# Kernel tuning notes

Measured on AMD Instinct MI355X. Metric: run time of the kernel, lower is better.

Reference implementation:

```python
import jax, jax.numpy as jnp
import numpy as np


def setup_inputs() -> dict:
    key = jax.random.key(0)
    k1, k2, k3, k4, k5 = jax.random.split(key, 5)
    B, ENS, XDIM, YDIM = 8, 256, 8192, 256
    return {
        "Ens_ten": jax.random.normal(k1, (B, ENS, XDIM), dtype=jnp.float32),
        "H": jax.random.normal(k2, (XDIM, YDIM), dtype=jnp.float32),
        "y_true_mean": jax.random.normal(k3, (1, YDIM), dtype=jnp.float32),
        "y_true_std": jax.random.normal(k4, (1, YDIM), dtype=jnp.float32),
        "noise": jax.random.normal(k5, (B, YDIM, ENS), dtype=jnp.float32),
    }


def reference(Ens_ten, H, y_true_mean, y_true_std, noise):
    # Ens_ten: [b, ens, xdim]; H: [xdim, ydim]
    b, ens, xdim = Ens_ten.shape
    Y = jnp.einsum('bex,xy->bey', Ens_ten, H)          # observation_func (linear)
    x_m = jnp.mean(Ens_ten, axis=1, keepdims=True)     # [b,1,xdim]
    y_m = jnp.mean(Y, axis=1, keepdims=True)           # [b,1,ydim]
    Xc = jnp.swapaxes(Ens_ten - x_m, 1, 2)             # [b,xdim,ens]
    Yc = jnp.swapaxes(Y - y_m, 1, 2)                   # [b,ydim,ens]
    C_xy = jnp.einsum('bxe,bye->bxy', Xc, Yc) / ens    # [b,xdim,ydim]
    C_yy = jnp.einsum('bue,bve->buv', Yc, Yc) / ens    # [b,ydim,ydim]
    R = jnp.diag(jnp.square(y_true_std)[0])            # [ydim,ydim], broadcasts over batch
    A = R + C_yy                                       # [b,ydim,ydim]
    # torch.linalg.solve(A, C_xy, left=False): K = C_xy @ inv(A)
    K = jnp.swapaxes(
        jnp.linalg.solve(jnp.swapaxes(A, 1, 2), jnp.swapaxes(C_xy, 1, 2)), 1, 2
    )                                                  # [b,xdim,ydim]
    R_2 = noise * jnp.square(y_true_std)[:, :, None]   # [b,ydim,ens]
    innov = y_true_mean[:, :, None] - Yc + R_2         # [b,ydim,ens]
    update = jnp.einsum('bxy,bye->bxe', K, innov)      # [b,xdim,ens]
    return Ens_ten + jnp.swapaxes(update, 1, 2)
```

## Files before the change

### kernel.cpp

```cpp
#include <hip/hip_runtime.h>

#define ENSN 256
#define XDIM 8192
#define YD 256
#define BATCH 8

#define OFF_Y   0
#define OFF_YC  524288
#define OFF_AUG 1048576
#define OFF_W   2097152
#define OFF_XM  2621440

typedef __attribute__((ext_vector_type(4))) short short4v;
typedef __attribute__((ext_vector_type(8))) short short8v;
typedef __attribute__((ext_vector_type(4))) float float4v;

__device__ __forceinline__ unsigned short f2bf_rne(float x) {
    unsigned u = __float_as_uint(x);
    u += 0x7FFFu + ((u >> 16) & 1u);
    return (unsigned short)(u >> 16);
}

__global__ __launch_bounds__(256) void k1_colmean(const float* __restrict__ E,
                                                  float* __restrict__ xm) {
    int x = blockIdx.x * 256 + threadIdx.x;
    int b = blockIdx.y;
    const float* p = E + (size_t)b * ENSN * XDIM + x;
    float s = 0.f;
    #pragma unroll 8
    for (int e = 0; e < ENSN; e++) s += p[(size_t)e * XDIM];
    xm[b * XDIM + x] = s * (1.0f / ENSN);
}

__global__ __launch_bounds__(256) void kc_h(const float* __restrict__ H,
                                            short* __restrict__ Hthi,
                                            short* __restrict__ Htlo) {
    __shared__ float T[64][65];
    int k0 = blockIdx.x * 64, n0 = blockIdx.y * 64;
    int tid = threadIdx.x;
    int c = tid & 63, g = tid >> 6;
    #pragma unroll
    for (int p = 0; p < 16; p++)
        T[g + p * 4][c] = H[(size_t)(k0 + g + p * 4) * YD + n0 + c];
    __syncthreads();
    #pragma unroll
    for (int p = 0; p < 16; p++) {
        int nn = g + p * 4;
        float v = T[c][nn];
        unsigned short h = f2bf_rne(v);
        float hf = __uint_as_float(((unsigned)h) << 16);
        unsigned short l2 = f2bf_rne(v - hf);
        Hthi[(size_t)(n0 + nn) * XDIM + k0 + c] = (short)h;
        Htlo[(size_t)(n0 + nn) * XDIM + k0 + c] = (short)l2;
    }
}

#define EST 40
#define BST 40

__global__ __launch_bounds__(512, 2) void k2m_ygemm(const float* __restrict__ E,
                                                    const short* __restrict__ Hthi,
                                                    const short* __restrict__ Htlo,
                                                    float* __restrict__ Y) {
    __shared__ __align__(16) short Ehi[64 * EST];
    __shared__ __align__(16) short Elo[64 * EST];
    __shared__ __align__(16) short Bhi[256 * BST];
    __shared__ __align__(16) short Blo[256 * BST];
    int tid = threadIdx.x;
    int lane = tid & 63;
    int w = tid >> 6;
    int m0 = blockIdx.x * 64;
    int kb0 = blockIdx.y * 512;
    int wr = (w & 1) * 32;
    int wc = (w >> 1) * 64;
    float4v acc[8];
    #pragma unroll
    for (int i = 0; i < 8; i++) acc[i] = (float4v){0.f, 0.f, 0.f, 0.f};

    int erow = tid >> 3, ecol = (tid & 7) * 4;
    int brow4 = tid >> 2, bch = (tid & 3) * 8;
    int fr = lane & 15, fg = lane >> 4;

    for (int s = 0; s < 16; s++) {
        int kb = kb0 + s * 32;
        float4 ev = *(const float4*)&E[(size_t)(m0 + erow) * XDIM + kb + ecol];
        float vv[4] = {ev.x, ev.y, ev.z, ev.w};
        short4v hi4, lo4;
        #pragma unroll
        for (int j = 0; j < 4; j++) {
            unsigned short h = f2bf_rne(vv[j]);
            float hf = __uint_as_float(((unsigned)h) << 16);
            unsigned short l2 = f2bf_rne(vv[j] - hf);
            hi4[j] = (short)h; lo4[j] = (short)l2;
        }
        *(short4v*)&Ehi[erow * EST + ecol] = hi4;
        *(short4v*)&Elo[erow * EST + ecol] = lo4;
        #pragma unroll
        for (int pass = 0; pass < 2; pass++) {
            int rowb = brow4 + pass * 128;
            *(short8v*)&Bhi[rowb * BST + bch] =
                *(const short8v*)&Hthi[(size_t)rowb * XDIM + kb + bch];
            *(short8v*)&Blo[rowb * BST + bch] =
                *(const short8v*)&Htlo[(size_t)rowb * XDIM + kb + bch];
        }
        __syncthreads();
        short8v ah[2], al[2], bhf[4], blf[4];
        #pragma unroll
        for (int ti = 0; ti < 2; ti++) {
            ah[ti] = *(const short8v*)&Ehi[(wr + ti * 16 + fr) * EST + fg * 8];
            al[ti] = *(const short8v*)&Elo[(wr + ti * 16 + fr) * EST + fg * 8];
        }
        #pragma unroll
        for (int tj = 0; tj < 4; tj++) {
            bhf[tj] = *(const short8v*)&Bhi[(wc + tj * 16 + fr) * BST + fg * 8];
            blf[tj] = *(const short8v*)&Blo[(wc + tj * 16 + fr) * BST + fg * 8];
        }
        #pragma unroll
        for (int ti = 0; ti < 2; ti++)
            #pragma unroll
            for (int tj = 0; tj < 4; tj++) {
                int a = ti * 4 + tj;
                acc[a] = __builtin_amdgcn_mfma_f32_16x16x32_bf16(ah[ti], bhf[tj], acc[a], 0, 0, 0);
                acc[a] = __builtin_amdgcn_mfma_f32_16x16x32_bf16(ah[ti], blf[tj], acc[a], 0, 0, 0);
                acc[a] = __builtin_amdgcn_mfma_f32_16x16x32_bf16(al[ti], bhf[tj], acc[a], 0, 0, 0);
            }
        __syncthreads();
    }
    #pragma unroll
    for (int ti = 0; ti < 2; ti++)
        #pragma unroll
        for (int tj = 0; tj < 4; tj++)
            #pragma unroll
            for (int q = 0; q < 4; q++) {
                int row = m0 + wr + ti * 16 + fg * 4 + q;
                int col = wc + tj * 16 + fr;
                atomicAdd(&Y[row * YD + col], acc[ti * 4 + tj][q]);
            }
}

__global__ __launch_bounds__(256) void k3_center(const float* __restrict__ Y,
                                                 const float* __restrict__ ytm,
                                                 const float* __restrict__ ystd,
                                                 const float* __restrict__ noise,
                                                 float* __restrict__ Yc,
                                                 float* __restrict__ aug) {
    int b = blockIdx.y, tid = threadIdx.x;
    int y0 = blockIdx.x * 64;
    __shared__ float red[4][64];
    __shared__ float ym[64], tms[64], s2[64];
    __shared__ float T[64][65];
    int yl = tid & 63, q = tid >> 6;
    float s = 0.f;
    for (int e = q * 64; e < q * 64 + 64; e++)
        s += Y[(size_t)(b * ENSN + e) * YD + y0 + yl];
    red[q][yl] = s;
    __syncthreads();
    if (tid < 64) {
        ym[tid] = (red[0][tid] + red[1][tid] + red[2][tid] + red[3][tid]) * (1.0f / ENSN);
        float sd = ystd[y0 + tid];
        s2[tid] = sd * sd;
        tms[tid] = ytm[y0 + tid];
    }
    __syncthreads();
    for (int e0 = 0; e0 < ENSN; e0 += 64) {
        #pragma unroll
        for (int p = 0; p < 16; p++) {
            int er = q + p * 4;
            T[er][yl] = Y[(size_t)(b * ENSN + e0 + er) * YD + y0 + yl];
        }
        __syncthreads();
        int ec = yl;
        #pragma unroll
        for (int p = 0; p < 16; p++) {
            int yr = q + p * 4;
            int y = y0 + yr, e = e0 + ec;
            float yv = T[ec][yr] - ym[yr];
            Yc[(size_t)b * YD * ENSN + (size_t)y * ENSN + e] = yv;
            aug[(size_t)b * YD * 512 + (size_t)y * 512 + 256 + e] =
                tms[yr] - yv + noise[(size_t)b * YD * ENSN + (size_t)y * ENSN + e] * s2[yr];
        }
        __syncthreads();
    }
}

__global__ __launch_bounds__(256) void k4_cyy(const float* __restrict__ Yc,
                                              const float* __restrict__ ystd,
                                              float* __restrict__ aug) {
    __shared__ float As[16][68];
    __shared__ float Bs[16][68];
    int tid = threadIdx.x;
    int m0 = blockIdx.x * 64, n0 = blockIdx.y * 64, b = blockIdx.z;
    const float* Ycb = Yc + (size_t)b * YD * ENSN;
    int tr = tid >> 4, tc = tid & 15;
    float acc[4][4];
    #pragma unroll
    for (int i = 0; i < 4; i++)
        #pragma unroll
        for (int j = 0; j < 4; j++) acc[i][j] = 0.f;
    int al = tid & 15, am0 = tid >> 4;
    for (int k0 = 0; k0 < ENSN; k0 += 16) {
        #pragma unroll
        for (int p = 0; p < 4; p++) {
            int am = am0 + p * 16;
            As[al][am] = Ycb[(m0 + am) * ENSN + k0 + al];
            Bs[al][am] = Ycb[(n0 + am) * ENSN + k0 + al];
        }
        __syncthreads();
        #pragma unroll
        for (int kk = 0; kk < 16; kk++) {
            float4 a = *(const float4*)&As[kk][tr * 4];
            float4 bb = *(const float4*)&Bs[kk][tc * 4];
            float af[4] = {a.x, a.y, a.z, a.w};
            float bf[4] = {bb.x, bb.y, bb.z, bb.w};
            #pragma unroll
            for (int i = 0; i < 4; i++)
                #pragma unroll
                for (int j = 0; j < 4; j++) acc[i][j] += af[i] * bf[j];
        }
        __syncthreads();
    }
    float* augb = aug + (size_t)b * YD * 512;
    #pragma unroll
    for (int i = 0; i < 4; i++) {
        int u = m0 + tr * 4 + i;
        #pragma unroll
        for (int j = 0; j < 4; j++) {
            int v = n0 + tc * 4 + j;
            float val = acc[i][j] * (1.0f / ENSN);
            if (u == v) { float sv = ystd[u]; val += sv * sv; }
            augb[u * 512 + v] = val;
        }
    }
}

#define RSTP 484
#define LSTP 233

__global__ __launch_bounds__(1024, 4) void k5p_panel(float* __restrict__ aug, int c0) {
    __shared__ __align__(16) float R[32 * RSTP];
    __shared__ float Ls[32 * LSTP];
    __shared__ __align__(16) float Dg[32 * 33];
    __shared__ float invd[32];
    int b = blockIdx.x, tid = threadIdx.x;
    float* A = aug + (size_t)b * 256 * 512;
    int r5 = tid >> 5, c5 = tid & 31;
    int WR = 480 - c0;
    int W2 = 224 - c0;

    Dg[r5 * 33 + c5] = A[(c0 + r5) * 512 + c0 + c5];
    __syncthreads();
    if (tid < 32) {
        float u[32];
        #pragma unroll
        for (int c = 0; c < 32; c++) u[c] = Dg[tid * 33 + c];
        for (int j = 0; j < 31; j++) {
            float pv = __shfl(u[j], j);
            float f = u[j] / pv;
            #pragma unroll
            for (int c = 0; c < 32; c++) {
                if (c > j) {
                    float ujc = __shfl(u[c], j);
                    if (tid > j) u[c] -= f * ujc;
                }
            }
            if (tid > j) u[j] = f;
        }
        #pragma unroll
        for (int c = 0; c < 32; c++) Dg[tid * 33 + c] = u[c];
        invd[tid] = 1.0f / u[tid];
    }
    for (int cc = c5; cc < WR; cc += 32)
        R[r5 * RSTP + cc] = A[(c0 + r5) * 512 + c0 + 32 + cc];
    for (int row = r5; row < W2; row += 32)
        Ls[c5 * LSTP + row] = A[(c0 + 32 + row) * 512 + c0 + c5];
    __syncthreads();
    A[(c0 + r5) * 512 + c0 + c5] = Dg[r5 * 33 + c5];
    if (tid < WR) {
        float y[32];
        #pragma unroll
        for (int j = 0; j < 32; j++) {
            float s = R[j * RSTP + tid];
            #pragma unroll
            for (int m = 0; m < 32; m++)
                if (m < j) s -= Dg[j * 33 + m] * y[m];
            y[j] = s;
        }
        #pragma unroll
        for (int j = 0; j < 32; j++)
            A[(c0 + j) * 512 + c0 + 32 + tid] = y[j];
    }
    if (tid >= 512 && tid < 512 + W2) {
        int row = tid - 512;
        float l[32];
        #pragma unroll
        for (int j = 0; j < 32; j++) {
            float s = Ls[j * LSTP + row];
            #pragma unroll
            for (int m = 0; m < 32; m++)
                if (m < j) s -= l[m] * Dg[m * 33 + j];
            l[j] = s * invd[j];
        }
        #pragma unroll
        for (int j = 0; j < 32; j++)
            Ls[j * LSTP + row] = l[j];
    }
    __syncthreads();
    for (int row = r5; row < W2; row += 32)
        A[(c0 + 32 + row) * 512 + c0 + c5] = Ls[c5 * LSTP + row];
}

__global__ __launch_bounds__(256) void k5t_trail(float* __restrict__ aug, int c0) {
    __shared__ __align__(16) float Lt[32][36];
    __shared__ __align__(16) float Ut[32][36];
    int b = blockIdx.z, tid = threadIdx.x;
    float* A = aug + (size_t)b * 256 * 512;
    int r0  = c0 + 32 + blockIdx.x * 32;
    int cc0 = c0 + 32 + blockIdx.y * 32;
    int lr = tid >> 3, lc = (tid & 7) * 4;
    *(float4*)&Lt[lr][lc] = *(const float4*)&A[(size_t)(r0 + lr) * 512 + c0 + lc];
    *(float4*)&Ut[lr][lc] = *(const float4*)&A[(size_t)(c0 + lr) * 512 + cc0 + lc];
    __syncthreads();
    float* gp = &A[(size_t)(r0 + lr) * 512 + cc0 + lc];
    float4 acc = *(const float4*)gp;
    #pragma unroll
    for (int k = 0; k < 32; k++) {
        float lv = Lt[lr][k];
        float4 uv = *(const float4*)&Ut[k][lc];
        acc.x -= lv * uv.x;
        acc.y -= lv * uv.y;
        acc.z -= lv * uv.z;
        acc.w -= lv * uv.w;
    }
    *(float4*)gp = acc;
}

__global__ __launch_bounds__(64) void k5i_invu(const float* __restrict__ aug,
                                               float* __restrict__ invU) {
    __shared__ float Dg[32 * 33];
    __shared__ float invd[32];
    int p = blockIdx.x, b = blockIdx.y, tid = threadIdx.x;
    const float* A = aug + (size_t)b * 256 * 512;
    int c0 = 32 * p;
    for (int i = tid; i < 1024; i += 64)
        Dg[(i >> 5) * 33 + (i & 31)] = A[(size_t)(c0 + (i >> 5)) * 512 + c0 + (i & 31)];
    __syncthreads();
    if (tid < 32) invd[tid] = 1.0f / Dg[tid * 33 + tid];
    __syncthreads();
    if (tid < 32) {
        int c = tid;
        float x[32];
        #pragma unroll
        for (int j = 31; j >= 0; j--) {
            float s = (j == c) ? 1.0f : 0.0f;
            #pragma unroll
            for (int m = 0; m < 32; m++)
                if (m > j) s -= Dg[j * 33 + m] * x[m];
            x[j] = s * invd[j];
        }
        float* op = invU + (size_t)(b * 8 + p) * 1024;
        #pragma unroll
        for (int j = 0; j < 32; j++) op[j * 32 + c] = x[j];
    }
}

#define ZST  36
#define LBST 36

__global__ __launch_bounds__(512, 2) void k5s_solve(float* __restrict__ aug,
                                                    const float* __restrict__ invU) {
    __shared__ __align__(16) float Zs[256 * ZST];
    __shared__ __align__(16) float Lb[224 * LBST];
    __shared__ __align__(16) float Dg[32 * 33];
    int b = blockIdx.y, tid = threadIdx.x;
    float* A = aug + (size_t)b * 256 * 512;
    int cb = blockIdx.x * 32;
    int c = tid & 31, g = tid >> 5;
    int rr = tid >> 5, cc = tid & 31;

    for (int r = g; r < 256; r += 16)
        Zs[r * ZST + c] = A[r * 512 + 256 + cb + c];

    for (int p = 7; p >= 0; p--) {
        int c0 = 32 * p, na = c0;
        for (int i = tid; i < 1024; i += 512)
            Dg[(i >> 5) * 33 + (i & 31)] = invU[(size_t)(b * 8 + p) * 1024 + i];
        for (int r = rr; r < na; r += 16)
            Lb[r * LBST + cc] = A[r * 512 + c0 + cc];
        __syncthreads();
        float z[32];
        #pragma unroll
        for (int m = 0; m < 32; m++) z[m] = Zs[(c0 + m) * ZST + c];
        float xr[2];
        #pragma unroll
        for (int r2 = 0; r2 < 2; r2++) {
            const float* dr = &Dg[(g * 2 + r2) * 33];
            float s0 = 0.f, s1 = 0.f, s2 = 0.f, s3 = 0.f;
            #pragma unroll
            for (int m = 0; m < 32; m += 4) {
                s0 += dr[m + 0] * z[m + 0];
                s1 += dr[m + 1] * z[m + 1];
                s2 += dr[m + 2] * z[m + 2];
                s3 += dr[m + 3] * z[m + 3];
            }
            xr[r2] = (s0 + s1) + (s2 + s3);
        }
        __syncthreads();
        #pragma unroll
        for (int r2 = 0; r2 < 2; r2++)
            Zs[(c0 + g * 2 + r2) * ZST + c] = xr[r2];
        __syncthreads();
        if (na > 0) {
            float zx[32];
            #pragma unroll
            for (int k = 0; k < 32; k++) zx[k] = Zs[(c0 + k) * ZST + c];
            for (int r = g; r < na; r += 16) {
                const float* lp = &Lb[r * LBST];
                float a0 = 0.f, a1 = 0.f, a2 = 0.f, a3 = 0.f;
                #pragma unroll
                for (int k = 0; k < 32; k += 4) {
                    float4 lv = *(const float4*)(lp + k);
                    a0 += lv.x * zx[k + 0];
                    a1 += lv.y * zx[k + 1];
                    a2 += lv.z * zx[k + 2];
                    a3 += lv.w * zx[k + 3];
                }
                Zs[r * ZST + c] -= (a0 + a1) + (a2 + a3);
            }
        }
        __syncthreads();
    }

    for (int r = g; r < 256; r += 16)
        A[r * 512 + 256 + cb + c] = Zs[r * ZST + c];
}

__global__ __launch_bounds__(256) void k6_w(const float* __restrict__ Yc,
                                            const float* __restrict__ aug,
                                            float* __restrict__ W) {
    __shared__ float As[16][68];
    __shared__ float Bs[16][68];
    int tid = threadIdx.x;
    int m0 = blockIdx.x * 64, n0 = blockIdx.y * 64, b = blockIdx.z;
    const float* Ycb = Yc + (size_t)b * YD * ENSN;
    const float* augb = aug + (size_t)b * YD * 512;
    int tr = tid >> 4, tc = tid & 15;
    float acc[4][4];
    #pragma unroll
    for (int i = 0; i < 4; i++)
        #pragma unroll
        for (int j = 0; j < 4; j++) acc[i][j] = 0.f;
    int c = tid & 63, kr0 = tid >> 6;
    for (int k0 = 0; k0 < YD; k0 += 16) {
        #pragma unroll
        for (int p = 0; p < 4; p++) {
            int kk = kr0 + p * 4;
            As[kk][c] = Ycb[(k0 + kk) * ENSN + m0 + c];
            Bs[kk][c] = augb[(k0 + kk) * 512 + 256 + n0 + c];
        }
        __syncthreads();
        #pragma unroll
        for (int kk = 0; kk < 16; kk++) {
            float4 a = *(const float4*)&As[kk][tr * 4];
            float4 bb = *(const float4*)&Bs[kk][tc * 4];
            float af[4] = {a.x, a.y, a.z, a.w};
            float bf[4] = {bb.x, bb.y, bb.z, bb.w};
            #pragma unroll
            for (int i = 0; i < 4; i++)
                #pragma unroll
                for (int j = 0; j < 4; j++) acc[i][j] += af[i] * bf[j];
        }
        __syncthreads();
    }
    float* Wb = W + (size_t)b * ENSN * ENSN;
    #pragma unroll
    for (int i = 0; i < 4; i++)
        #pragma unroll
        for (int j = 0; j < 4; j++)
            Wb[(m0 + tr * 4 + i) * ENSN + n0 + tc * 4 + j] = acc[i][j] * (1.0f / ENSN);
}

__global__ __launch_bounds__(256) void kw_w(const float* __restrict__ W,
                                            short* __restrict__ Wthi,
                                            short* __restrict__ Wtlo) {
    __shared__ float T[64][65];
    int f0 = blockIdx.x * 64, e0 = blockIdx.y * 64, b = blockIdx.z;
    const float* Wb = W + (size_t)b * ENSN * ENSN;
    int tid = threadIdx.x;
    int c = tid & 63, g = tid >> 6;
    #pragma unroll
    for (int p = 0; p < 16; p++)
        T[g + p * 4][c] = Wb[(size_t)(f0 + g + p * 4) * ENSN + e0 + c];
    __syncthreads();
    #pragma unroll
    for (int p = 0; p < 16; p++) {
        int ee = g + p * 4;
        float v = T[c][ee];
        unsigned short h = f2bf_rne(v);
        float hf = __uint_as_float(((unsigned)h) << 16);
        unsigned short l2 = f2bf_rne(v - hf);
        size_t o = (size_t)b * ENSN * ENSN + (size_t)(e0 + ee) * ENSN + f0 + c;
        Wthi[o] = (short)h;
        Wtlo[o] = (short)l2;
    }
}

#define WST 36
#define XST 36

__global__ __launch_bounds__(512, 2) void k7m_update(const float* __restrict__ E,
                                                     const short* __restrict__ Wthi,
                                                     const short* __restrict__ Wtlo,
                                                     const float* __restrict__ xm,
                                                     float* __restrict__ out) {
    __shared__ __align__(16) short Ahi[256 * WST];
    __shared__ __align__(16) short Alo[256 * WST];
    __shared__ __align__(16) short Bhi[64 * XST];
    __shared__ __align__(16) short Blo[64 * XST];
    __shared__ float xs[64];
    int tid = threadIdx.x;
    int lane = tid & 63;
    int w = tid >> 6;
    int x0 = blockIdx.x * 64;
    int b = blockIdx.y;
    const short* Whb = Wthi + (size_t)b * ENSN * ENSN;
    const short* Wlb = Wtlo + (size_t)b * ENSN * ENSN;
    const float* Eb = E + (size_t)b * ENSN * XDIM;
    if (tid < 64) xs[tid] = xm[b * XDIM + x0 + tid];
    __syncthreads();
    int wr = (w & 3) * 64;
    int wc = (w >> 2) * 32;
    float4v acc[8];
    #pragma unroll
    for (int i = 0; i < 8; i++) acc[i] = (float4v){0.f, 0.f, 0.f, 0.f};
    int fr = lane & 15, fg = lane >> 4;
    int ae = tid >> 2, ach = (tid & 3) * 8;
    int bx = tid & 63, bkq = tid >> 6;

    for (int s = 0; s < 8; s++) {
        int k0 = s * 32;
        #pragma unroll
        for (int h = 0; h < 2; h++) {
            int e = ae + h * 128;
            *(short8v*)&Ahi[e * WST + ach] = *(const short8v*)&Whb[(size_t)e * ENSN + k0 + ach];
            *(short8v*)&Alo[e * WST + ach] = *(const short8v*)&Wlb[(size_t)e * ENSN + k0 + ach];
        }
        short4v hi4, lo4;
        #pragma unroll
        for (int j = 0; j < 4; j++) {
            float v = Eb[(size_t)(k0 + bkq * 4 + j) * XDIM + x0 + bx] - xs[bx];
            unsigned short h = f2bf_rne(v);
            float hf = __uint_as_float(((unsigned)h) << 16);
            unsigned short l2 = f2bf_rne(v - hf);
            hi4[j] = (short)h; lo4[j] = (short)l2;
        }
        *(short4v*)&Bhi[bx * XST + bkq * 4] = hi4;
        *(short4v*)&Blo[bx * XST + bkq * 4] = lo4;
        __syncthreads();
        short8v ah[4], al[4], bhf[2], blf[2];
        #pragma unroll
        for (int ti = 0; ti < 4; ti++) {
            ah[ti] = *(const short8v*)&Ahi[(wr + ti * 16 + fr) * WST + fg * 8];
            al[ti] = *(const short8v*)&Alo[(wr + ti * 16 + fr) * WST + fg * 8];
        }
        #pragma unroll
        for (int tj = 0; tj < 2; tj++) {
            bhf[tj] = *(const short8v*)&Bhi[(wc + tj * 16 + fr) * XST + fg * 8];
            blf[tj] = *(const short8v*)&Blo[(wc + tj * 16 + fr) * XST + fg * 8];
        }
        #pragma unroll
        for (int ti = 0; ti < 4; ti++)
            #pragma unroll
            for (int tj = 0; tj < 2; tj++) {
                int a = ti * 2 + tj;
                acc[a] = __builtin_amdgcn_mfma_f32_16x16x32_bf16(ah[ti], bhf[tj], acc[a], 0, 0, 0);
                acc[a] = __builtin_amdgcn_mfma_f32_16x16x32_bf16(ah[ti], blf[tj], acc[a], 0, 0, 0);
                acc[a] = __builtin_amdgcn_mfma_f32_16x16x32_bf16(al[ti], bhf[tj], acc[a], 0, 0, 0);
            }
        __syncthreads();
    }
    #pragma unroll
    for (int ti = 0; ti < 4; ti++)
        #pragma unroll
        for (int tj = 0; tj < 2; tj++)
            #pragma unroll
            for (int q = 0; q < 4; q++) {
                int e = wr + ti * 16 + fg * 4 + q;
                int x = x0 + wc + tj * 16 + fr;
                size_t idx = (size_t)(b * ENSN + e) * XDIM + x;
                out[idx] = E[idx] + acc[ti * 2 + tj][q];
            }
}

extern "C" void kernel_launch(void* const* d_in, const int* in_sizes, int n_in,
                              void* d_out, int out_size, void* d_ws, size_t ws_size,
                              hipStream_t stream) {
    const float* Ens   = (const float*)d_in[0];
    const float* H     = (const float*)d_in[1];
    const float* ytm   = (const float*)d_in[2];
    const float* ystd  = (const float*)d_in[3];
    const float* noise = (const float*)d_in[4];
    float* out = (float*)d_out;
    float* ws  = (float*)d_ws;

    float* Y   = ws + OFF_Y;
    float* Yc  = ws + OFF_YC;
    float* aug = ws + OFF_AUG;
    float* W   = ws + OFF_W;
    float* xm  = ws + OFF_XM;
    short* Hthi = (short*)(ws + 524288);
    short* Htlo = (short*)(ws + 1572864);
    short* Wthi = (short*)(ws + 0);
    short* Wtlo = (short*)(ws + 262144);
    float* invU = ws + OFF_W;

    hipMemsetAsync(Y, 0, (size_t)2048 * 256 * sizeof(float), stream);

    k1_colmean<<<dim3(XDIM / 256, BATCH), 256, 0, stream>>>(Ens, xm);
    kc_h<<<dim3(XDIM / 64, YD / 64), 256, 0, stream>>>(H, Hthi, Htlo);
    k2m_ygemm<<<dim3(2048 / 64, 16), 512, 0, stream>>>(Ens, Hthi, Htlo, Y);
    k3_center<<<dim3(4, BATCH), 256, 0, stream>>>(Y, ytm, ystd, noise, Yc, aug);
    k4_cyy<<<dim3(4, 4, BATCH), 256, 0, stream>>>(Yc, ystd, aug);
    for (int p = 0; p < 8; p++) {
        k5p_panel<<<dim3(BATCH), 1024, 0, stream>>>(aug, 32 * p);
        if (p < 7)
            k5t_trail<<<dim3(7 - p, 15 - p, BATCH), 256, 0, stream>>>(aug, 32 * p);
    }
    k5i_invu<<<dim3(8, BATCH), 64, 0, stream>>>(aug, invU);
    k5s_solve<<<dim3(8, BATCH), 512, 0, stream>>>(aug, invU);
    k6_w<<<dim3(4, 4, BATCH), 256, 0, stream>>>(Yc, aug, W);
    kw_w<<<dim3(4, 4, BATCH), 256, 0, stream>>>(W, Wthi, Wtlo);
    k7m_update<<<dim3(XDIM / 64, BATCH), 512, 0, stream>>>(Ens, Wthi, Wtlo, xm, out);
}
```

Before: 644.5 us.

## Store GEMM tiles in MFMA fragment order in LDS and double k2 split-K

The Y-GEMM and update kernels now write their shared-memory tiles in the exact fragment order the MFMA instructions consume. Each lane then reads its operand with one contiguous 16-byte load instead of using padded row-stride indexing. The Y-GEMM split-K factor goes from 16 to 32, and the occupancy hints in the launch bounds are raised on both kernels. The aim is fewer LDS bank conflicts and more parallel blocks. The cost is more atomic partial sums into Y and possibly more register pressure from the higher occupancy targets.

```diff
diff --git a/kernel.cpp b/kernel.cpp
--- a/kernel.cpp
+++ b/kernel.cpp
@@ -55,22 +55,22 @@
     }
 }
 
-#define EST 40
-#define BST 40
-
-__global__ __launch_bounds__(512, 2) void k2m_ygemm(const float* __restrict__ E,
+#define K2SPLIT 32
+#define K2KB    (XDIM / K2SPLIT)
+
+__global__ __launch_bounds__(512, 8) void k2m_ygemm(const float* __restrict__ E,
                                                     const short* __restrict__ Hthi,
                                                     const short* __restrict__ Htlo,
                                                     float* __restrict__ Y) {
-    __shared__ __align__(16) short Ehi[64 * EST];
-    __shared__ __align__(16) short Elo[64 * EST];
-    __shared__ __align__(16) short Bhi[256 * BST];
-    __shared__ __align__(16) short Blo[256 * BST];
+    __shared__ __align__(16) short Efh[4 * 64 * 8];
+    __shared__ __align__(16) short Efl[4 * 64 * 8];
+    __shared__ __align__(16) short Bfh[16 * 64 * 8];
+    __shared__ __align__(16) short Bfl[16 * 64 * 8];
     int tid = threadIdx.x;
     int lane = tid & 63;
     int w = tid >> 6;
     int m0 = blockIdx.x * 64;
-    int kb0 = blockIdx.y * 512;
+    int kb0 = blockIdx.y * K2KB;
     int wr = (w & 1) * 32;
     int wc = (w >> 1) * 64;
     float4v acc[8];
@@ -78,10 +78,14 @@
     for (int i = 0; i < 8; i++) acc[i] = (float4v){0.f, 0.f, 0.f, 0.f};
 
     int erow = tid >> 3, ecol = (tid & 7) * 4;
-    int brow4 = tid >> 2, bch = (tid & 3) * 8;
+    int efg = (tid & 7) >> 1, ehalf = tid & 1;
+    int ebase = (((erow >> 4) * 64 + efg * 16 + (erow & 15)) << 3) + ehalf * 4;
+    int brow = tid >> 1, bf0 = (tid & 1) * 2;
+    int bbase0 = (((brow >> 4) * 64 + (bf0 + 0) * 16 + (brow & 15)) << 3);
+    int bbase1 = (((brow >> 4) * 64 + (bf0 + 1) * 16 + (brow & 15)) << 3);
     int fr = lane & 15, fg = lane >> 4;
 
-    for (int s = 0; s < 16; s++) {
+    for (int s = 0; s < K2KB / 32; s++) {
         int kb = kb0 + s * 32;
         float4 ev = *(const float4*)&E[(size_t)(m0 + erow) * XDIM + kb + ecol];
         float vv[4] = {ev.x, ev.y, ev.z, ev.w};
@@ -93,27 +97,29 @@
             unsigned short l2 = f2bf_rne(vv[j] - hf);
             hi4[j] = (short)h; lo4[j] = (short)l2;
         }
-        *(short4v*)&Ehi[erow * EST + ecol] = hi4;
-        *(short4v*)&Elo[erow * EST + ecol] = lo4;
-        #pragma unroll
-        for (int pass = 0; pass < 2; pass++) {
-            int rowb = brow4 + pass * 128;
-            *(short8v*)&Bhi[rowb * BST + bch] =
-                *(const short8v*)&Hthi[(size_t)rowb * XDIM + kb + bch];
-            *(short8v*)&Blo[rowb * BST + bch] =
-                *(const short8v*)&Htlo[(size_t)rowb * XDIM + kb + bch];
-        }
+        *(short4v*)&Efh[ebase] = hi4;
+        *(short4v*)&Efl[ebase] = lo4;
+        short8v bh0 = *(const short8v*)&Hthi[(size_t)brow * XDIM + kb + bf0 * 8];
+        short8v bh1 = *(const short8v*)&Hthi[(size_t)brow * XDIM + kb + bf0 * 8 + 8];
+        short8v bl0 = *(const short8v*)&Htlo[(size_t)brow * XDIM + kb + bf0 * 8];
+        short8v bl1 = *(const short8v*)&Htlo[(size_t)brow * XDIM + kb + bf0 * 8 + 8];
+        *(short8v*)&Bfh[bbase0] = bh0;
+        *(short8v*)&Bfh[bbase1] = bh1;
+        *(short8v*)&Bfl[bbase0] = bl0;
+        *(short8v*)&Bfl[bbase1] = bl1;
         __syncthreads();
         short8v ah[2], al[2], bhf[4], blf[4];
         #pragma unroll
         for (int ti = 0; ti < 2; ti++) {
-            ah[ti] = *(const short8v*)&Ehi[(wr + ti * 16 + fr) * EST + fg * 8];
-            al[ti] = *(const short8v*)&Elo[(wr + ti * 16 + fr) * EST + fg * 8];
+            int t = ((wr >> 4) + ti) * 512 + lane * 8;
+            ah[ti] = *(const short8v*)&Efh[t];
+            al[ti] = *(const short8v*)&Efl[t];
         }
         #pragma unroll
         for (int tj = 0; tj < 4; tj++) {
-            bhf[tj] = *(const short8v*)&Bhi[(wc + tj * 16 + fr) * BST + fg * 8];
-            blf[tj] = *(const short8v*)&Blo[(wc + tj * 16 + fr) * BST + fg * 8];
+            int t = ((wc >> 4) + tj) * 512 + lane * 8;
+            bhf[tj] = *(const short8v*)&Bfh[t];
+            blf[tj] = *(const short8v*)&Bfl[t];
         }
         #pragma unroll
         for (int ti = 0; ti < 2; ti++)
@@ -504,18 +510,15 @@
     }
 }
 
-#define WST 36
-#define XST 36
-
-__global__ __launch_bounds__(512, 2) void k7m_update(const float* __restrict__ E,
+__global__ __launch_bounds__(512, 4) void k7m_update(const float* __restrict__ E,
                                                      const short* __restrict__ Wthi,
                                                      const short* __restrict__ Wtlo,
                                                      const float* __restrict__ xm,
                                                      float* __restrict__ out) {
-    __shared__ __align__(16) short Ahi[256 * WST];
-    __shared__ __align__(16) short Alo[256 * WST];
-    __shared__ __align__(16) short Bhi[64 * XST];
-    __shared__ __align__(16) short Blo[64 * XST];
+    __shared__ __align__(16) short Afh[16 * 64 * 8];
+    __shared__ __align__(16) short Afl[16 * 64 * 8];
+    __shared__ __align__(16) short Bfh[4 * 64 * 8];
+    __shared__ __align__(16) short Bfl[4 * 64 * 8];
     __shared__ float xs[64];
     int tid = threadIdx.x;
     int lane = tid & 63;
@@ -533,17 +536,19 @@
     #pragma unroll
     for (int i = 0; i < 8; i++) acc[i] = (float4v){0.f, 0.f, 0.f, 0.f};
     int fr = lane & 15, fg = lane >> 4;
-    int ae = tid >> 2, ach = (tid & 3) * 8;
+    int arow = tid >> 1, af0 = (tid & 1) * 2;
+    int abase0 = (((arow >> 4) * 64 + (af0 + 0) * 16 + (arow & 15)) << 3);
+    int abase1 = (((arow >> 4) * 64 + (af0 + 1) * 16 + (arow & 15)) << 3);
     int bx = tid & 63, bkq = tid >> 6;
+    int bfg = bkq >> 1, bhalf = bkq & 1;
+    int bbase = (((bx >> 4) * 64 + bfg * 16 + (bx & 15)) << 3) + bhalf * 4;
 
     for (int s = 0; s < 8; s++) {
         int k0 = s * 32;
-        #pragma unroll
-        for (int h = 0; h < 2; h++) {
-            int e = ae + h * 128;
-            *(short8v*)&Ahi[e * WST + ach] = *(const short8v*)&Whb[(size_t)e * ENSN + k0 + ach];
-            *(short8v*)&Alo[e * WST + ach] = *(const short8v*)&Wlb[(size_t)e * ENSN + k0 + ach];
-        }
+        *(short8v*)&Afh[abase0] = *(const short8v*)&Whb[(size_t)arow * ENSN + k0 + af0 * 8];
+        *(short8v*)&Afh[abase1] = *(const short8v*)&Whb[(size_t)arow * ENSN + k0 + af0 * 8 + 8];
+        *(short8v*)&Afl[abase0] = *(const short8v*)&Wlb[(size_t)arow * ENSN + k0 + af0 * 8];
+        *(short8v*)&Afl[abase1] = *(const short8v*)&Wlb[(size_t)arow * ENSN + k0 + af0 * 8 + 8];
         short4v hi4, lo4;
         #pragma unroll
         for (int j = 0; j < 4; j++) {
@@ -553,19 +558,21 @@
             unsigned short l2 = f2bf_rne(v - hf);
             hi4[j] = (short)h; lo4[j] = (short)l2;
         }
-        *(short4v*)&Bhi[bx * XST + bkq * 4] = hi4;
-        *(short4v*)&Blo[bx * XST + bkq * 4] = lo4;
+        *(short4v*)&Bfh[bbase] = hi4;
+        *(short4v*)&Bfl[bbase] = lo4;
         __syncthreads();
         short8v ah[4], al[4], bhf[2], blf[2];
         #pragma unroll
         for (int ti = 0; ti < 4; ti++) {
-            ah[ti] = *(const short8v*)&Ahi[(wr + ti * 16 + fr) * WST + fg * 8];
-            al[ti] = *(const short8v*)&Alo[(wr + ti * 16 + fr) * WST + fg * 8];
+            int t = ((wr >> 4) + ti) * 512 + lane * 8;
+            ah[ti] = *(const short8v*)&Afh[t];
+            al[ti] = *(const short8v*)&Afl[t];
         }
         #pragma unroll
         for (int tj = 0; tj < 2; tj++) {
-            bhf[tj] = *(const short8v*)&Bhi[(wc + tj * 16 + fr) * XST + fg * 8];
-            blf[tj] = *(const short8v*)&Blo[(wc + tj * 16 + fr) * XST + fg * 8];
+            int t = ((wc >> 4) + tj) * 512 + lane * 8;
+            bhf[tj] = *(const short8v*)&Bfh[t];
+            blf[tj] = *(const short8v*)&Bfl[t];
         }
         #pragma unroll
         for (int ti = 0; ti < 4; ti++)
@@ -617,7 +624,7 @@
 
     k1_colmean<<<dim3(XDIM / 256, BATCH), 256, 0, stream>>>(Ens, xm);
     kc_h<<<dim3(XDIM / 64, YD / 64), 256, 0, stream>>>(H, Hthi, Htlo);
-    k2m_ygemm<<<dim3(2048 / 64, 16), 512, 0, stream>>>(Ens, Hthi, Htlo, Y);
+    k2m_ygemm<<<dim3(2048 / 64, K2SPLIT), 512, 0, stream>>>(Ens, Hthi, Htlo, Y);
     k3_center<<<dim3(4, BATCH), 256, 0, stream>>>(Y, ytm, ystd, noise, Yc, aug);
     k4_cyy<<<dim3(4, 4, BATCH), 256, 0, stream>>>(Yc, ystd, aug);
     for (int p = 0; p < 8; p++) {
```

Result: slower. 734.4 us (+14.0%).
